# Optimization experiments

Measured on AMD Instinct MI355X. Metric: run time of the kernel, lower is better.

Reference implementation:

```python
import jax, jax.numpy as jnp
import numpy as np

N = 1000   # node count forced by fc1_1 in_features=1680 (see shape derivation)
E = 8000   # edges, avg degree ~8
F_IN = 6   # node feature dim (first 3 = pos, zeroed in forward)


def setup_inputs() -> dict:
    key = jax.random.key(0)
    ks = jax.random.split(key, 24)
    f = lambda k, s, sc=1.0: jax.random.normal(k, s, dtype=jnp.float32) * sc
    inp = {
        "x": f(ks[0], (N, F_IN)),
        "edge_index": jax.random.randint(ks[1], (2, E), 0, N, dtype=jnp.int64),
        # GCNConv weights (xavier-ish scale)
        "W1": f(ks[2], (F_IN, 32), 0.4), "b1": jnp.zeros((32,), jnp.float32),
        "W2": f(ks[3], (32, 32), 0.18), "b2": jnp.zeros((32,), jnp.float32),
        # Conv2d kernels, OIHW
        "k1": f(ks[4], (3, 1, 3, 2), 0.3), "kb1": jnp.zeros((3,), jnp.float32),
        "k2": f(ks[5], (6, 3, 3, 2), 0.2), "kb2": jnp.zeros((6,), jnp.float32),
        "k3": f(ks[6], (3, 6, 3, 2), 0.2), "kb3": jnp.zeros((3,), jnp.float32),
        "k4": f(ks[7], (1, 3, 3, 2), 0.2), "kb4": jnp.zeros((1,), jnp.float32),
        # FC head (torch Linear layout: [out, in])
        "fw1": f(ks[8], (1024, 1680), 0.02), "fb1": jnp.zeros((1024,), jnp.float32),
        "fw2": f(ks[9], (1024, 1024), 0.03), "fb2": jnp.zeros((1024,), jnp.float32),
        "fw3": f(ks[10], (64, 1024), 0.03), "fb3": jnp.zeros((64,), jnp.float32),
    }
    return inp


def _conv2d(x, w, b):
    out = jax.lax.conv_general_dilated(
        x, w, window_strides=(1, 1), padding="VALID",
        dimension_numbers=("NCHW", "OIHW", "NCHW"))
    return out + b[None, :, None, None]


def _maxpool2(x):  # MaxPool2d((2,1), stride=(2,1))
    return jax.lax.reduce_window(x, -jnp.inf, jax.lax.max,
                                 (1, 1, 2, 1), (1, 1, 2, 1), "VALID")


def reference(x, edge_index, W1, b1, W2, b2, k1, kb1, k2, kb2, k3, kb3, k4, kb4,
              fw1, fb1, fw2, fb2, fw3, fb3):
    num_nodes = x.shape[0]
    # forward zeroes the first 3 features (positions)
    x = x.at[:, :3].set(0.0)

    loop = jnp.arange(num_nodes)
    row = jnp.concatenate([edge_index[0], loop])
    col = jnp.concatenate([edge_index[1], loop])
    deg = jnp.zeros((num_nodes,), x.dtype).at[col].add(1.0)
    dinv = jnp.where(deg > 0, jax.lax.rsqrt(deg), 0.0)
    norm = (dinv[row] * dinv[col])[:, None]  # [E+N, 1]

    def gcn(h, W, b):
        hw = h @ W                                   # [N, 32]
        msg = hw[row] * norm                         # gather + scale
        return jax.ops.segment_sum(msg, col, num_segments=num_nodes) + b

    leaky = lambda v: jnp.where(v > 0, v, 0.2 * v)   # LeakyReLU(0.2)
    h = leaky(gcn(x, W1, b1))
    h = leaky(gcn(h, W2, b2))                        # [N, 32]

    img = h[None, None]                              # [1, 1, N, 32]
    img = _maxpool2(jax.nn.relu(_conv2d(img, k1, kb1)))   # [1,3,499,31]
    img = _maxpool2(jax.nn.relu(_conv2d(img, k2, kb2)))   # [1,6,248,30]
    img = _maxpool2(jax.nn.relu(_conv2d(img, k3, kb3)))   # [1,3,123,29]
    img = _maxpool2(jax.nn.relu(_conv2d(img, k4, kb4)))   # [1,1,60,28]

    v = img.reshape(-1)                              # [1680]
    v = v @ fw1.T + fb1                              # no activation between FCs (as in source)
    v = v @ fw2.T + fb2
    v = v @ fw3.T + fb3                              # [64]
    return v
```

## Files before the change

kernel.cpp:

```cpp
#include <hip/hip_runtime.h>

#define LEAKY(v) ((v) > 0.0f ? (v) : 0.2f * (v))

__global__ __launch_bounds__(256) void kA_prep(
        const int* __restrict__ col, const float* __restrict__ fw2,
        const float* __restrict__ fw3, float* __restrict__ deg,
        float* __restrict__ aggs ,
        float* __restrict__ Mpart, int n, int E) {
    int T = blockIdx.x * 256 + (int)threadIdx.x;
    if (T < 2 * n * 32) aggs[T] = 0.0f;
    int wave = T >> 6, lane = T & 63;
    if (wave < n) {
        int cnt = 0;
        for (int e = lane; e < E; e += 64) cnt += (col[e] == wave) ? 1 : 0;
#pragma unroll
        for (int off = 32; off > 0; off >>= 1) cnt += __shfl_down(cnt, off, 64);
        if (lane == 0) deg[wave] = (float)cnt;
    }
    {
        int jc = blockIdx.x >> 4;
        int it = (blockIdx.x & 15) * 64;
        int w  = (int)threadIdx.x >> 6;
        int i  = it + ((int)threadIdx.x & 63);
        int j0 = jc * 64;
        float acc[16];
#pragma unroll
        for (int kk = 0; kk < 16; ++kk) acc[kk] = 0.0f;
        const float* f3 = fw3 + (size_t)(w * 16) * 1024 + j0;
        for (int jj = 0; jj < 64; ++jj) {
            float wv = fw2[(size_t)(j0 + jj) * 1024 + i];
#pragma unroll
            for (int kk = 0; kk < 16; ++kk)
                acc[kk] += f3[(size_t)kk * 1024 + jj] * wv;
        }
#pragma unroll
        for (int kk = 0; kk < 16; ++kk)
            Mpart[(size_t)(jc * 64 + w * 16 + kk) * 1024 + i] = acc[kk];
    }
}

__global__ void kB_scatter1(const float* __restrict__ x, const float* __restrict__ W1,
        const float* __restrict__ deg, const int* __restrict__ row,
        const int* __restrict__ col, float* __restrict__ agg1, int E, int n) {
    int tid = blockIdx.x * blockDim.x + threadIdx.x;
    int total = (E + n) * 32;
    if (tid >= total) return;
    int e = tid >> 5, j = tid & 31;
    int r, c; float nrm;
    if (e < E) {
        r = row[e]; c = col[e];
        nrm = (1.0f / sqrtf(deg[r] + 1.0f)) * (1.0f / sqrtf(deg[c] + 1.0f));
    } else {
        r = c = e - E;
        nrm = 1.0f / (deg[r] + 1.0f);
    }
    float val = x[r*6+3] * W1[96+j] + x[r*6+4] * W1[128+j] + x[r*6+5] * W1[160+j];
    atomicAdd(&agg1[c * 32 + j], val * nrm);
}

__global__ void kC_scatter2(const float* __restrict__ agg1, const float* __restrict__ b1,
        const float* __restrict__ W2, const float* __restrict__ deg,
        const int* __restrict__ row, const int* __restrict__ col,
        float* __restrict__ agg2, int E, int n) {
    int tid = blockIdx.x * blockDim.x + threadIdx.x;
    int total = (E + n) * 32;
    if (tid >= total) return;
    int e = tid >> 5, j = tid & 31;
    int r, c; float nrm;
    if (e < E) {
        r = row[e]; c = col[e];
        nrm = (1.0f / sqrtf(deg[r] + 1.0f)) * (1.0f / sqrtf(deg[c] + 1.0f));
    } else {
        r = c = e - E;
        nrm = 1.0f / (deg[r] + 1.0f);
    }
    const float* a = agg1 + r * 32;
    float s = 0.0f;
#pragma unroll
    for (int f = 0; f < 32; ++f) {
        float v = a[f] + b1[f];
        v = LEAKY(v);
        s += v * W2[f * 32 + j];
    }
    atomicAdd(&agg2[c * 32 + j], s * nrm);
}

__global__ __launch_bounds__(256) void kD_c3(const float* __restrict__ agg2,
        const float* __restrict__ b2,
        const float* __restrict__ k1w, const float* __restrict__ kb1,
        const float* __restrict__ k2w, const float* __restrict__ kb2,
        const float* __restrict__ k3w, const float* __restrict__ kb3,
        float* __restrict__ c3) {
    __shared__ float lc1[3][10][31];
    __shared__ float lc2[6][4][30];
    const int oh3 = blockIdx.x;
    const int tid = (int)threadIdx.x;

    for (int idx = tid; idx < 930; idx += 256) {
        int ci = idx / 310, rem = idx % 310;
        int hh = rem / 31, ow1 = rem % 31;
        int r0 = (4 * oh3 + hh) * 2;
        const float* kw = k1w + ci * 6;
        float v[4][2];
#pragma unroll
        for (int rr = 0; rr < 4; ++rr)
#pragma unroll
            for (int dc = 0; dc < 2; ++dc) {
                float u = agg2[(r0 + rr) * 32 + ow1 + dc] + b2[ow1 + dc];
                v[rr][dc] = LEAKY(u);
            }
        float a0 = v[0][0]*kw[0] + v[0][1]*kw[1] + v[1][0]*kw[2]
                 + v[1][1]*kw[3] + v[2][0]*kw[4] + v[2][1]*kw[5];
        float a1 = v[1][0]*kw[0] + v[1][1]*kw[1] + v[2][0]*kw[2]
                 + v[2][1]*kw[3] + v[3][0]*kw[4] + v[3][1]*kw[5];
        lc1[ci][hh][ow1] = fmaxf(fmaxf(a0, a1) + kb1[ci], 0.0f);
    }
    __syncthreads();

    for (int idx = tid; idx < 720; idx += 256) {
        int co2 = idx / 120, rem = idx % 120;
        int r = rem / 30, ow2 = rem % 30;
        float p0 = 0.0f, p1 = 0.0f;
#pragma unroll
        for (int ci = 0; ci < 3; ++ci) {
            const float* kw = k2w + (co2 * 3 + ci) * 6;
            const float* q0 = &lc1[ci][2*r][ow2];
            float r00 = q0[0],      r01 = q0[1];
            float r10 = q0[31],     r11 = q0[32];
            float r20 = q0[62],     r21 = q0[63];
            float r30 = q0[93],     r31 = q0[94];
            p0 += r00*kw[0] + r01*kw[1] + r10*kw[2] + r11*kw[3] + r20*kw[4] + r21*kw[5];
            p1 += r10*kw[0] + r11*kw[1] + r20*kw[2] + r21*kw[3] + r30*kw[4] + r31*kw[5];
        }
        lc2[co2][r][ow2] = fmaxf(fmaxf(p0, p1) + kb2[co2], 0.0f);
    }
    __syncthreads();

    if (tid < 87) {
        int co = tid / 29, ow3 = tid % 29;
        float A0 = 0.0f, A1 = 0.0f;
#pragma unroll
        for (int co2 = 0; co2 < 6; ++co2) {
            const float* kw3 = k3w + (co * 6 + co2) * 6;
            const float* q0 = &lc2[co2][0][ow3];
            float r00 = q0[0],      r01 = q0[1];
            float r10 = q0[30],     r11 = q0[31];
            float r20 = q0[60],     r21 = q0[61];
            float r30 = q0[90],     r31 = q0[91];
            A0 += r00*kw3[0] + r01*kw3[1] + r10*kw3[2] + r11*kw3[3] + r20*kw3[4] + r21*kw3[5];
            A1 += r10*kw3[0] + r11*kw3[1] + r20*kw3[2] + r21*kw3[3] + r30*kw3[4] + r31*kw3[5];
        }
        c3[(co * 123 + oh3) * 29 + ow3] = fmaxf(fmaxf(A0, A1) + kb3[co], 0.0f);
    }
}

__global__ __launch_bounds__(256) void kE_conv4_fc1(
        const float* __restrict__ c3, const float* __restrict__ k4,
        const float* __restrict__ kb4, const float* __restrict__ fw1,
        const float* __restrict__ fb1, float* __restrict__ f1) {
    __shared__ __align__(16) float lc4[1680];
    const int Hin = 123, Win = 29, Wo = 28;
    float kb = kb4[0];
    for (int t0 = (int)threadIdx.x; t0 < 1680; t0 += 256) {
        int ow = t0 % Wo; int oh = t0 / Wo;
        float a0 = 0.0f, a1 = 0.0f;
#pragma unroll
        for (int ci = 0; ci < 3; ++ci) {
            const float* q = c3 + (ci * Hin + 2 * oh) * Win + ow;
            const float* wp = k4 + ci * 6;
            float r00 = q[0],     r01 = q[1];
            float r10 = q[Win],   r11 = q[Win+1];
            float r20 = q[2*Win], r21 = q[2*Win+1];
            float r30 = q[3*Win], r31 = q[3*Win+1];
            a0 += r00*wp[0] + r01*wp[1] + r10*wp[2] + r11*wp[3] + r20*wp[4] + r21*wp[5];
            a1 += r10*wp[0] + r11*wp[1] + r20*wp[2] + r21*wp[3] + r30*wp[4] + r31*wp[5];
        }
        float m = fmaxf(a0, a1) + kb;
        lc4[t0] = fmaxf(m, 0.0f);
    }
    __syncthreads();
    int wv = (int)threadIdx.x >> 6, lane = (int)threadIdx.x & 63;
    int o = blockIdx.x * 4 + wv;
    const float4* wr = (const float4*)(fw1 + (size_t)o * 1680);
    const float4* vv = (const float4*)lc4;
    float s = 0.0f;
    for (int i = lane; i < 420; i += 64) {
        float4 a = vv[i], ww = wr[i];
        s += a.x*ww.x + a.y*ww.y + a.z*ww.z + a.w*ww.w;
    }
#pragma unroll
    for (int off = 32; off > 0; off >>= 1) s += __shfl_down(s, off, 64);
    if (lane == 0) f1[o] = s + fb1[o];
}

__global__ __launch_bounds__(256) void kF_head(const float* __restrict__ f1,
        const float* __restrict__ Mpart, const float* __restrict__ fw3,
        const float* __restrict__ fb2, const float* __restrict__ fb3,
        float* __restrict__ out) {
    int wv = (int)threadIdx.x >> 6, lane = (int)threadIdx.x & 63;
    int k = blockIdx.x * 4 + wv;
    const float4* vv = (const float4*)f1;
    const float4* f3 = (const float4*)(fw3 + (size_t)k * 1024);
    const float4* bb = (const float4*)fb2;
    float s = 0.0f;
#pragma unroll
    for (int i2 = 0; i2 < 4; ++i2) {
        float4 c = bb[lane + 64*i2], w3 = f3[lane + 64*i2];
        s += c.x*w3.x + c.y*w3.y + c.z*w3.z + c.w*w3.w;
    }
    for (int jc = 0; jc < 16; ++jc) {
        const float4* Mr = (const float4*)(Mpart + (size_t)(jc * 64 + k) * 1024);
#pragma unroll
        for (int i2 = 0; i2 < 4; ++i2) {
            float4 a = vv[lane + 64*i2], ww = Mr[lane + 64*i2];
            s += a.x*ww.x + a.y*ww.y + a.z*ww.z + a.w*ww.w;
        }
    }
#pragma unroll
    for (int off = 32; off > 0; off >>= 1) s += __shfl_down(s, off, 64);
    if (lane == 0) out[k] = s + fb3[k];
}

extern "C" void kernel_launch(void* const* d_in, const int* in_sizes, int n_in,
                              void* d_out, int out_size, void* d_ws, size_t ws_size,
                              hipStream_t stream) {
    const float* x   = (const float*)d_in[0];
    const int*   ei  = (const int*)d_in[1];
    const float* W1  = (const float*)d_in[2];
    const float* b1  = (const float*)d_in[3];
    const float* W2  = (const float*)d_in[4];
    const float* b2  = (const float*)d_in[5];
    const float* k1  = (const float*)d_in[6];
    const float* kb1 = (const float*)d_in[7];
    const float* k2  = (const float*)d_in[8];
    const float* kb2 = (const float*)d_in[9];
    const float* k3  = (const float*)d_in[10];
    const float* kb3 = (const float*)d_in[11];
    const float* k4  = (const float*)d_in[12];
    const float* kb4 = (const float*)d_in[13];
    const float* fw1 = (const float*)d_in[14];
    const float* fb1 = (const float*)d_in[15];
    const float* fw2 = (const float*)d_in[16];
    const float* fb2 = (const float*)d_in[17];
    const float* fw3 = (const float*)d_in[18];
    const float* fb3 = (const float*)d_in[19];

    int n = in_sizes[0] / 6;
    int E = in_sizes[1] / 2;
    const int* row = ei;
    const int* col = ei + E;

    float* ws    = (float*)d_ws;
    float* deg   = ws;
    float* agg1  = ws + 1024;
    float* agg2  = agg1 + 32000;
    float* Mpart = agg2 + 32000;
    float* c3    = Mpart + 1048576;
    float* f1    = c3 + 10704;

    const int B = 256;
    int st = (E + n) * 32;

    kA_prep<<<256, B, 0, stream>>>(col, fw2, fw3, deg, agg1, Mpart, n, E);
    kB_scatter1<<<(st + B - 1) / B, B, 0, stream>>>(x, W1, deg, row, col, agg1, E, n);
    kC_scatter2<<<(st + B - 1) / B, B, 0, stream>>>(agg1, b1, W2, deg, row, col, agg2, E, n);
    kD_c3<<<123, B, 0, stream>>>(agg2, b2, k1, kb1, k2, kb2, k3, kb3, c3);
    kE_conv4_fc1<<<256, B, 0, stream>>>(c3, k4, kb4, fw1, fb1, f1);
    kF_head<<<16, B, 0, stream>>>(f1, Mpart, fw3, fb2, fb3, (float*)d_out);
}
```

Measured before the change: 164.3 us.

## Drop precomputed fw3·fw2 product; compute fc2 and fc3 directly with atomics

Removes the per-call 64x1024x1024 product of fw3 and fw2 from the prep kernel and replaces the head with a kernel that computes fc2 as a GEMV and fc3 partial sums accumulated into the output via atomicAdd. The prep kernel now zeroes the output and counts degrees with one 256-thread block per node. This cuts roughly 67M FMAs and a 4MB intermediate write per call, at the cost of atomic, order-nondeterministic float accumulation in the output.

Result: faster. 156.7 us (-4.6%).

```diff
diff --git a/kernel.cpp b/kernel.cpp
--- a/kernel.cpp
+++ b/kernel.cpp
@@ -3,39 +3,25 @@
 #define LEAKY(v) ((v) > 0.0f ? (v) : 0.2f * (v))
 
 __global__ __launch_bounds__(256) void kA_prep(
-        const int* __restrict__ col, const float* __restrict__ fw2,
-        const float* __restrict__ fw3, float* __restrict__ deg,
+        const int* __restrict__ col, float* __restrict__ deg,
         float* __restrict__ aggs ,
-        float* __restrict__ Mpart, int n, int E) {
+        float* __restrict__ outz, int n, int E) {
     int T = blockIdx.x * 256 + (int)threadIdx.x;
-    if (T < 2 * n * 32) aggs[T] = 0.0f;
-    int wave = T >> 6, lane = T & 63;
-    if (wave < n) {
+    int nz = 2 * n * 32;
+    if (T < nz) aggs[T] = 0.0f;
+    else if (T < nz + 64) outz[T - nz] = 0.0f;
+
+    int b = blockIdx.x;
+    if (b < n) {
+        __shared__ int wsum[4];
+        int tid = (int)threadIdx.x;
         int cnt = 0;
-        for (int e = lane; e < E; e += 64) cnt += (col[e] == wave) ? 1 : 0;
+        for (int e = tid; e < E; e += 256) cnt += (col[e] == b) ? 1 : 0;
 #pragma unroll
         for (int off = 32; off > 0; off >>= 1) cnt += __shfl_down(cnt, off, 64);
-        if (lane == 0) deg[wave] = (float)cnt;
-    }
-    {
-        int jc = blockIdx.x >> 4;
-        int it = (blockIdx.x & 15) * 64;
-        int w  = (int)threadIdx.x >> 6;
-        int i  = it + ((int)threadIdx.x & 63);
-        int j0 = jc * 64;
-        float acc[16];
-#pragma unroll
-        for (int kk = 0; kk < 16; ++kk) acc[kk] = 0.0f;
-        const float* f3 = fw3 + (size_t)(w * 16) * 1024 + j0;
-        for (int jj = 0; jj < 64; ++jj) {
-            float wv = fw2[(size_t)(j0 + jj) * 1024 + i];
-#pragma unroll
-            for (int kk = 0; kk < 16; ++kk)
-                acc[kk] += f3[(size_t)kk * 1024 + jj] * wv;
-        }
-#pragma unroll
-        for (int kk = 0; kk < 16; ++kk)
-            Mpart[(size_t)(jc * 64 + w * 16 + kk) * 1024 + i] = acc[kk];
+        if ((tid & 63) == 0) wsum[tid >> 6] = cnt;
+        __syncthreads();
+        if (tid == 0) deg[b] = (float)(wsum[0] + wsum[1] + wsum[2] + wsum[3]);
     }
 }
 
@@ -193,32 +179,39 @@
     if (lane == 0) f1[o] = s + fb1[o];
 }
 
-__global__ __launch_bounds__(256) void kF_head(const float* __restrict__ f1,
-        const float* __restrict__ Mpart, const float* __restrict__ fw3,
-        const float* __restrict__ fb2, const float* __restrict__ fb3,
+__global__ __launch_bounds__(256) void kF_fc23(const float* __restrict__ f1,
+        const float* __restrict__ fw2, const float* __restrict__ fb2,
+        const float* __restrict__ fw3, const float* __restrict__ fb3,
         float* __restrict__ out) {
+    __shared__ float f2loc[16];
     int wv = (int)threadIdx.x >> 6, lane = (int)threadIdx.x & 63;
-    int k = blockIdx.x * 4 + wv;
+    int jbase = blockIdx.x * 16;
     const float4* vv = (const float4*)f1;
-    const float4* f3 = (const float4*)(fw3 + (size_t)k * 1024);
-    const float4* bb = (const float4*)fb2;
-    float s = 0.0f;
-#pragma unroll
-    for (int i2 = 0; i2 < 4; ++i2) {
-        float4 c = bb[lane + 64*i2], w3 = f3[lane + 64*i2];
-        s += c.x*w3.x + c.y*w3.y + c.z*w3.z + c.w*w3.w;
-    }
-    for (int jc = 0; jc < 16; ++jc) {
-        const float4* Mr = (const float4*)(Mpart + (size_t)(jc * 64 + k) * 1024);
+    for (int q = 0; q < 4; ++q) {
+        int j = jbase + wv * 4 + q;
+        const float4* wr = (const float4*)(fw2 + (size_t)j * 1024);
+        float s = 0.0f;
 #pragma unroll
         for (int i2 = 0; i2 < 4; ++i2) {
-            float4 a = vv[lane + 64*i2], ww = Mr[lane + 64*i2];
+            float4 a = vv[lane + 64*i2], ww = wr[lane + 64*i2];
             s += a.x*ww.x + a.y*ww.y + a.z*ww.z + a.w*ww.w;
         }
-    }
-#pragma unroll
-    for (int off = 32; off > 0; off >>= 1) s += __shfl_down(s, off, 64);
-    if (lane == 0) out[k] = s + fb3[k];
+#pragma unroll
+        for (int off = 32; off > 0; off >>= 1) s += __shfl_down(s, off, 64);
+        if (lane == 0) f2loc[wv * 4 + q] = s + fb2[j];
+    }
+    __syncthreads();
+    for (int kk = 0; kk < 16; ++kk) {
+        int k = wv * 16 + kk;
+        float v = 0.0f;
+        if (lane < 16) v = fw3[(size_t)k * 1024 + jbase + lane] * f2loc[lane];
+#pragma unroll
+        for (int off = 8; off > 0; off >>= 1) v += __shfl_down(v, off, 16);
+        if (lane == 0) {
+            if (blockIdx.x == 0) v += fb3[k];
+            atomicAdd(&out[k], v);
+        }
+    }
 }
 
 extern "C" void kernel_launch(void* const* d_in, const int* in_sizes, int n_in,
@@ -250,21 +243,20 @@
     const int* row = ei;
     const int* col = ei + E;
 
-    float* ws    = (float*)d_ws;
-    float* deg   = ws;
-    float* agg1  = ws + 1024;
-    float* agg2  = agg1 + 32000;
-    float* Mpart = agg2 + 32000;
-    float* c3    = Mpart + 1048576;
-    float* f1    = c3 + 10704;
+    float* ws   = (float*)d_ws;
+    float* deg  = ws;
+    float* agg1 = ws + 1024;
+    float* agg2 = agg1 + 32000;
+    float* c3   = agg2 + 32000;
+    float* f1   = c3 + 10704;
 
     const int B = 256;
     int st = (E + n) * 32;
 
-    kA_prep<<<256, B, 0, stream>>>(col, fw2, fw3, deg, agg1, Mpart, n, E);
+    kA_prep<<<n, B, 0, stream>>>(col, deg, agg1, (float*)d_out, n, E);
     kB_scatter1<<<(st + B - 1) / B, B, 0, stream>>>(x, W1, deg, row, col, agg1, E, n);
     kC_scatter2<<<(st + B - 1) / B, B, 0, stream>>>(agg1, b1, W2, deg, row, col, agg2, E, n);
     kD_c3<<<123, B, 0, stream>>>(agg2, b2, k1, kb1, k2, kb2, k3, kb3, c3);
     kE_conv4_fc1<<<256, B, 0, stream>>>(c3, k4, kb4, fw1, fb1, f1);
-    kF_head<<<16, B, 0, stream>>>(f1, Mpart, fw3, fb2, fb3, (float*)d_out);
-}
+    kF_fc23<<<64, B, 0, stream>>>(f1, fw2, fb2, fw3, fb3, (float*)d_out);
+}
```
